# Kernel optimization log

Measured on AMD Instinct MI355X. Metric: run time of the kernel, lower is better.

The kernel has to match this reference:

```python
import jax, jax.numpy as jnp
import numpy as np

B, S, D, H = 4, 2048, 1024, 16
DH = D // H


def setup_inputs() -> dict:
    key = jax.random.key(0)
    k1, k2, k3 = jax.random.split(key, 3)
    x = jax.random.normal(k1, (B, S, D), dtype=jnp.float32)
    w_attn = jax.random.normal(k2, (D, 3 * D), dtype=jnp.float32) * 0.02
    b_attn = jnp.zeros((3 * D,), dtype=jnp.float32)
    w_proj = jax.random.normal(k3, (D, D), dtype=jnp.float32) * 0.02
    b_proj = jnp.zeros((D,), dtype=jnp.float32)
    return {"x": x, "w_attn": w_attn, "b_attn": b_attn, "w_proj": w_proj, "b_proj": b_proj}


def _split_heads(t):
    # [B, S, D] -> [B, H, S, DH]
    return t.reshape(B, S, H, DH).transpose(0, 2, 1, 3)


def reference(x, w_attn, b_attn, w_proj, b_proj):
    # fused QKV projection (TFConv1D = x @ w + b)
    qkv = jnp.einsum('bsd,df->bsf', x, w_attn) + b_attn  # [B, S, 3D]
    q, k, v = jnp.split(qkv, 3, axis=2)
    q, k, v = _split_heads(q), _split_heads(k), _split_heads(v)  # [B,H,S,DH]

    # scaled scores
    w = jnp.einsum('bhqd,bhkd->bhqk', q, k) / jnp.sqrt(jnp.asarray(DH, dtype=q.dtype))

    # causal mask: multiply + additive -10000 trick, as in original
    i = jnp.arange(S)[:, None]
    j = jnp.arange(S)[None, :]
    b = (i >= j).astype(w.dtype)  # nd == ns so i >= j - ns + nd == i >= j
    b = b[None, None]  # [1,1,S,S]
    w = w * b - 10000.0 * (1.0 - b)

    w = jax.nn.softmax(w, axis=-1)
    # attn_pdrop = 0.0 -> dropout is identity (eval)

    a = jnp.einsum('bhqk,bhkd->bhqd', w, v)  # [B,H,S,DH]
    a = a.transpose(0, 2, 1, 3).reshape(B, S, D)  # merge heads
    a = jnp.einsum('bsd,df->bsf', a, w_proj) + b_proj
    # resid_pdrop = 0.0 -> identity
    return a
```

## Files before the change

### kernel.cpp

```cpp
#include <hip/hip_runtime.h>
#include <stdint.h>

typedef __bf16 bf16x8 __attribute__((ext_vector_type(8)));
typedef float  f32x4  __attribute__((ext_vector_type(4)));

#define DEV __device__ __forceinline__

constexpr int Bc = 4, S = 2048, D = 1024, Hh = 16, DH = 64;
constexpr int Kdim = 1024;

DEV unsigned short f2bf(float f) {
    uint32_t u = __builtin_bit_cast(uint32_t, f);
    u += 0x7fff + ((u >> 16) & 1);
    return (unsigned short)(u >> 16);
}
DEV bf16x8 ld8(const unsigned short* p) {
    uint4 u = *(const uint4*)p;
    return __builtin_bit_cast(bf16x8, u);
}
DEV uint4 pack8(float4 a, float4 b) {
    union { uint4 u; unsigned short s[8]; } r;
    r.s[0] = f2bf(a.x); r.s[1] = f2bf(a.y); r.s[2] = f2bf(a.z); r.s[3] = f2bf(a.w);
    r.s[4] = f2bf(b.x); r.s[5] = f2bf(b.y); r.s[6] = f2bf(b.z); r.s[7] = f2bf(b.w);
    return r.u;
}

DEV void gl16(const void* g, void* l) {
    __builtin_amdgcn_global_load_lds((__attribute__((address_space(1))) void*)g,
                                     (__attribute__((address_space(3))) void*)l,
                                     16, 0, 0);
}

__global__ __launch_bounds__(256) void transpose_cvt(const float* __restrict__ in,
                                                     unsigned short* __restrict__ out,
                                                     int rows, int cols) {
    __shared__ float t[32][33];
    int tx = threadIdx.x & 31, ty = threadIdx.x >> 5;
    int c = blockIdx.x * 32 + tx;
    int rbase = blockIdx.y * 32;
    for (int rr = 0; rr < 32; rr += 8)
        t[ty + rr][tx] = in[(size_t)(rbase + ty + rr) * cols + c];
    __syncthreads();
    int orbase = blockIdx.x * 32;
    for (int rr = 0; rr < 32; rr += 8)
        out[(size_t)(orbase + ty + rr) * rows + rbase + tx] = f2bf(t[tx][ty + rr]);
}

__global__ __launch_bounds__(256) void cvt_bf16(const float* __restrict__ in,
                                                unsigned short* __restrict__ out) {
    size_t i = (size_t)blockIdx.x * 256 + threadIdx.x;
    const float4* p = (const float4*)(in + i * 8);
    float4 a = p[0], b = p[1];
    *(uint4*)(out + i * 8) = pack8(a, b);
}

__global__ __launch_bounds__(256) void gemm_bt(const unsigned short* __restrict__ A,
                                               const unsigned short* __restrict__ Bt,
                                               const float* __restrict__ bias,
                                               int mode,
                                               unsigned short* __restrict__ qo,
                                               unsigned short* __restrict__ ko,
                                               unsigned short* __restrict__ vo,
                                               float* __restrict__ outf) {
    __shared__ __align__(16) unsigned short As[2][128 * 64];
    __shared__ __align__(16) unsigned short Bs[2][128 * 64];
    const int tid = threadIdx.x;
    const int wave = tid >> 6, lane = tid & 63, g = lane >> 4, ln = lane & 15;
    const int wm = wave >> 1, wn = wave & 1;
    const int nwg = gridDim.x * gridDim.y;
    const int orig = blockIdx.y * gridDim.x + blockIdx.x;
    const int swz = (orig & 7) * (nwg >> 3) + (orig >> 3);
    const int m0 = (swz / gridDim.x) * 128, n0 = (swz % gridDim.x) * 128;

    f32x4 acc[4][4];
    for (int i = 0; i < 4; i++)
        for (int j = 0; j < 4; j++) acc[i][j] = f32x4{0.f, 0.f, 0.f, 0.f};

#define STAGE_G(buf, k0)                                                            \
    _Pragma("unroll")                                                               \
    for (int c = 0; c < 4; c++) {                                                   \
        int L = c * 4096 + tid * 16;                                                \
        int row = L >> 7;                                                           \
        int colb = (L & 127) ^ ((row & 7) << 4);                                    \
        gl16((const char*)A  + ((size_t)(m0 + row) * Kdim + (k0)) * 2 + colb,       \
             (char*)As[buf] + c * 4096 + wave * 1024);                              \
        gl16((const char*)Bt + ((size_t)(n0 + row) * Kdim + (k0)) * 2 + colb,       \
             (char*)Bs[buf] + c * 4096 + wave * 1024);                              \
    }

    STAGE_G(0, 0);
    asm volatile("s_waitcnt vmcnt(0)" ::: "memory");
    __builtin_amdgcn_s_barrier();
    asm volatile("" ::: "memory");

#pragma unroll 1
    for (int t = 0; t < 16; t++) {
        const int buf = t & 1;
        if (t + 1 < 16) STAGE_G(buf ^ 1, (t + 1) * 64);
        const unsigned short* Asb = As[buf];
        const unsigned short* Bsb = Bs[buf];
#pragma unroll
        for (int kk = 0; kk < 2; kk++) {
            bf16x8 af[4], bfr[4];
#pragma unroll
            for (int u = 0; u < 4; u++) {
                int ra = wm * 64 + u * 16 + ln;
                int rb = wn * 64 + u * 16 + ln;
                int co = kk * 64 + g * 16;
                af[u]  = ld8((const unsigned short*)((const char*)Asb + ra * 128 + (co ^ ((ra & 7) << 4))));
                bfr[u] = ld8((const unsigned short*)((const char*)Bsb + rb * 128 + (co ^ ((rb & 7) << 4))));
            }
#pragma unroll
            for (int mt = 0; mt < 4; mt++)
#pragma unroll
                for (int nt = 0; nt < 4; nt++)
                    acc[mt][nt] = __builtin_amdgcn_mfma_f32_16x16x32_bf16(af[mt], bfr[nt], acc[mt][nt], 0, 0, 0);
        }
        asm volatile("" ::: "memory");
        asm volatile("s_waitcnt vmcnt(0)" ::: "memory");
        __builtin_amdgcn_s_barrier();
        asm volatile("" ::: "memory");
    }
#undef STAGE_G

    for (int mt = 0; mt < 4; mt++)
        for (int nt = 0; nt < 4; nt++)
            for (int r = 0; r < 4; r++) {
                int m = m0 + wm * 64 + mt * 16 + g * 4 + r;
                int n = n0 + wn * 64 + nt * 16 + ln;
                float val = acc[mt][nt][r] + bias[n];
                if (mode == 0) {
                    int which = n >> 10, rem = n & 1023;
                    int hh = rem >> 6, dd = rem & 63;
                    int b = m >> 11, s = m & 2047;
                    int bh = (b << 4) + hh;
                    if (which == 0)      qo[((size_t)bh * S + s) * DH + dd] = f2bf(val);
                    else if (which == 1) ko[((size_t)bh * S + s) * DH + dd] = f2bf(val);
                    else                 vo[((size_t)bh * DH + dd) * S + s] = f2bf(val);
                } else {
                    outf[(size_t)m * 1024 + n] = val;
                }
            }
}

__global__ __launch_bounds__(512, 4) void attn_fwd(const unsigned short* __restrict__ qg,
                                                   const unsigned short* __restrict__ kg,
                                                   const unsigned short* __restrict__ vtg,
                                                   unsigned short* __restrict__ og) {
    __shared__ __align__(16) unsigned short Ks[128 * 64];
    __shared__ __align__(16) unsigned short Vs[64 * 128];
    __shared__ __align__(16) unsigned short P [128 * 136];
    const int idx = blockIdx.x;
    const int qt = 15 - (idx >> 6);
    const int bh = idx & 63;
    const int b = bh >> 4, h = bh & 15;
    const size_t base = (size_t)bh * S * DH;
    const unsigned short* qp = qg + base;
    const char* kpb  = (const char*)(kg  + base);
    const char* vtpb = (const char*)(vtg + base);
    const int tid = threadIdx.x, wave = tid >> 6, lane = tid & 63;
    const int g = lane >> 4, ln = lane & 15;
    const int q0 = qt * 128, wq = wave * 16;
    const int jn = qt + 1;

    bf16x8 qf[2];
    qf[0] = ld8(qp + (size_t)(q0 + wq + ln) * DH + g * 8);
    qf[1] = ld8(qp + (size_t)(q0 + wq + ln) * DH + 32 + g * 8);

    f32x4 o_t[4];
#pragma unroll
    for (int dt = 0; dt < 4; dt++) o_t[dt] = f32x4{0.f, 0.f, 0.f, 0.f};
    float m_ = -1e30f, l_ = 0.f;

#pragma unroll 1
    for (int j = 0; j < jn; j++) {
        const char* kj = kpb + (size_t)j * (128 * DH * 2);
        const char* vj = vtpb + j * 256;
#pragma unroll
        for (int c = 0; c < 2; c++) {
            int L = c * 8192 + tid * 16;
            int kr = L >> 7, kcb = L & 127;
            gl16(kj + (size_t)kr * 128 + (kcb ^ ((kr & 7) << 4)),
                 (char*)Ks + c * 8192 + wave * 1024);
            int vr = L >> 8, vcb = L & 255;
            gl16(vj + (size_t)vr * 4096 + (vcb ^ ((vr & 15) << 4)),
                 (char*)Vs + c * 8192 + wave * 1024);
        }
        __syncthreads();

        f32x4 st[8];
#pragma unroll
        for (int mt = 0; mt < 8; mt++) {
            int row = mt * 16 + ln;
            int sw = (row & 7) << 4;
            const char* kb2 = (const char*)Ks + row * 128;
            bf16x8 kf0 = ld8((const unsigned short*)(kb2 + ((g * 16) ^ sw)));
            bf16x8 kf1 = ld8((const unsigned short*)(kb2 + ((64 + g * 16) ^ sw)));
            f32x4 t = f32x4{0.f, 0.f, 0.f, 0.f};
            t = __builtin_amdgcn_mfma_f32_16x16x32_bf16(kf0, qf[0], t, 0, 0, 0);
            t = __builtin_amdgcn_mfma_f32_16x16x32_bf16(kf1, qf[1], t, 0, 0, 0);
            st[mt] = t;
        }
        if (j == jn - 1) {
            int qgl = q0 + wq + ln;
#pragma unroll
            for (int mt = 0; mt < 8; mt++)
#pragma unroll
                for (int r = 0; r < 4; r++) {
                    int kvg = j * 128 + mt * 16 + g * 4 + r;
                    if (kvg > qgl) st[mt][r] = -3e38f;
                }
        }
        f32x4 mm = st[0];
#pragma unroll
        for (int mt = 1; mt < 8; mt++)
#pragma unroll
            for (int e = 0; e < 4; e++) mm[e] = fmaxf(mm[e], st[mt][e]);
        float mx = fmaxf(fmaxf(mm[0], mm[1]), fmaxf(mm[2], mm[3]));
        mx = fmaxf(mx, __shfl_xor(mx, 16));
        mx = fmaxf(mx, __shfl_xor(mx, 32));
        float mnew = fmaxf(m_, mx);
        float alpha = __expf((m_ - mnew) * 0.125f);
        f32x4 sv = f32x4{0.f, 0.f, 0.f, 0.f};
#pragma unroll
        for (int mt = 0; mt < 8; mt++) {
            f32x4 pr;
#pragma unroll
            for (int e = 0; e < 4; e++) pr[e] = __expf((st[mt][e] - mnew) * 0.125f);
            st[mt] = pr;
            sv += pr;
        }
        float rs = (sv[0] + sv[1]) + (sv[2] + sv[3]);
        rs += __shfl_xor(rs, 16);
        rs += __shfl_xor(rs, 32);
        l_ = l_ * alpha + rs;
        m_ = mnew;

#pragma unroll
        for (int mt = 0; mt < 8; mt++) {
            uint4 u = __builtin_bit_cast(uint4, st[mt]);
            uint2 w;
            w.x = (u.y & 0xFFFF0000u) | (u.x >> 16);
            w.y = (u.w & 0xFFFF0000u) | (u.z >> 16);
            *(uint2*)&P[(wq + ln) * 136 + mt * 16 + g * 4] = w;
        }
#pragma unroll
        for (int dt = 0; dt < 4; dt++) o_t[dt] *= alpha;

#pragma unroll
        for (int kc = 0; kc < 4; kc++) {
            bf16x8 pf = ld8(&P[(wq + ln) * 136 + kc * 32 + g * 8]);
            bf16x8 vf[4];
#pragma unroll
            for (int dt = 0; dt < 4; dt++) {
                int row = dt * 16 + ln;
                vf[dt] = ld8((const unsigned short*)((const char*)Vs + row * 256 +
                             ((kc * 64 + g * 16) ^ ((row & 15) << 4))));
            }
#pragma unroll
            for (int dt = 0; dt < 4; dt++)
                o_t[dt] = __builtin_amdgcn_mfma_f32_16x16x32_bf16(vf[dt], pf, o_t[dt], 0, 0, 0);
        }
        __syncthreads();
    }

    float il = 1.f / l_;
#pragma unroll
    for (int dt = 0; dt < 4; dt++) o_t[dt] *= il;
    float* Ot = (float*)&P[wq * 136];
#pragma unroll
    for (int dt = 0; dt < 4; dt++)
        *(float4*)&Ot[ln * 68 + dt * 16 + g * 4] =
            float4{o_t[dt][0], o_t[dt][1], o_t[dt][2], o_t[dt][3]};
#pragma unroll
    for (int i = 0; i < 4; i++) {
        float4 v = *(float4*)&Ot[(i * 4 + g) * 68 + ln * 4];
        uint2 w;
        w.x = (uint32_t)f2bf(v.x) | ((uint32_t)f2bf(v.y) << 16);
        w.y = (uint32_t)f2bf(v.z) | ((uint32_t)f2bf(v.w) << 16);
        *(uint2*)&og[((size_t)(b * S + q0 + wq + i * 4 + g)) * D + h * DH + ln * 4] = w;
    }
}

extern "C" void kernel_launch(void* const* d_in, const int* in_sizes, int n_in,
                              void* d_out, int out_size, void* d_ws, size_t ws_size,
                              hipStream_t stream) {
    (void)in_sizes; (void)n_in; (void)out_size; (void)ws_size;
    const float* x      = (const float*)d_in[0];
    const float* w_attn = (const float*)d_in[1];
    const float* b_attn = (const float*)d_in[2];
    const float* w_proj = (const float*)d_in[3];
    const float* b_proj = (const float*)d_in[4];

    char* ws = (char*)d_ws;
    unsigned short* wattn_t = (unsigned short*)ws;
    unsigned short* wproj_t = (unsigned short*)(ws + 6291456);
    unsigned short* xb      = (unsigned short*)(ws + 8388608);
    unsigned short* qb      = (unsigned short*)(ws + 25165824);
    unsigned short* kb      = (unsigned short*)(ws + 41943040);
    unsigned short* vtb     = (unsigned short*)(ws + 58720256);
    unsigned short* aob     = (unsigned short*)(ws + 75497472);

    transpose_cvt<<<dim3(96, 32), 256, 0, stream>>>(w_attn, wattn_t, 1024, 3072);
    transpose_cvt<<<dim3(32, 32), 256, 0, stream>>>(w_proj, wproj_t, 1024, 1024);
    cvt_bf16<<<dim3(4096), 256, 0, stream>>>(x, xb);
    gemm_bt<<<dim3(24, 64), 256, 0, stream>>>(xb, wattn_t, b_attn, 0, qb, kb, vtb, nullptr);
    attn_fwd<<<dim3(1024), 512, 0, stream>>>(qb, kb, vtb, aob);
    gemm_bt<<<dim3(8, 64), 256, 0, stream>>>(aob, wproj_t, b_proj, 1,
                                             nullptr, nullptr, nullptr, (float*)d_out);
}
```

Measured before the change: 264.5 us.

## Restructure GEMM into 128x256 tiles with 8 waves and triple-buffered split staging

The GEMM tile grows from 128x128 with 4 waves to 128x256 with 8 waves, and LDS moves to a triple buffer that prefetches two K-steps ahead. The B-tile global loads are split into two halves issued at different points in the iteration, and each MFMA phase is wrapped in s_setprio. The aim is to hide global-load latency and raise MFMA density per barrier. In exchange the block uses more LDS (144KB), the grid shrinks to half as many blocks (especially small for the projection GEMM: 256 blocks), and the vmcnt bookkeeping becomes delicate.

```diff
diff --git a/kernel.cpp b/kernel.cpp
--- a/kernel.cpp
+++ b/kernel.cpp
@@ -54,81 +54,142 @@
     *(uint4*)(out + i * 8) = pack8(a, b);
 }
 
-__global__ __launch_bounds__(256) void gemm_bt(const unsigned short* __restrict__ A,
-                                               const unsigned short* __restrict__ Bt,
-                                               const float* __restrict__ bias,
-                                               int mode,
-                                               unsigned short* __restrict__ qo,
-                                               unsigned short* __restrict__ ko,
-                                               unsigned short* __restrict__ vo,
-                                               float* __restrict__ outf) {
-    __shared__ __align__(16) unsigned short As[2][128 * 64];
-    __shared__ __align__(16) unsigned short Bs[2][128 * 64];
+__global__ __launch_bounds__(512, 2) void gemm_bt(const unsigned short* __restrict__ A,
+                                                  const unsigned short* __restrict__ Bt,
+                                                  const float* __restrict__ bias,
+                                                  int mode,
+                                                  unsigned short* __restrict__ qo,
+                                                  unsigned short* __restrict__ ko,
+                                                  unsigned short* __restrict__ vo,
+                                                  float* __restrict__ outf) {
+    __shared__ __align__(16) unsigned short As[3][128 * 64];
+    __shared__ __align__(16) unsigned short Bs[3][256 * 64];
     const int tid = threadIdx.x;
     const int wave = tid >> 6, lane = tid & 63, g = lane >> 4, ln = lane & 15;
-    const int wm = wave >> 1, wn = wave & 1;
+    const int wm = wave >> 2, wn = wave & 3;
     const int nwg = gridDim.x * gridDim.y;
     const int orig = blockIdx.y * gridDim.x + blockIdx.x;
     const int swz = (orig & 7) * (nwg >> 3) + (orig >> 3);
-    const int m0 = (swz / gridDim.x) * 128, n0 = (swz % gridDim.x) * 128;
+    const int m0 = (swz / gridDim.x) * 128, n0 = (swz % gridDim.x) * 256;
 
     f32x4 acc[4][4];
     for (int i = 0; i < 4; i++)
         for (int j = 0; j < 4; j++) acc[i][j] = f32x4{0.f, 0.f, 0.f, 0.f};
 
-#define STAGE_G(buf, k0)                                                            \
+#define STAGE_A(buf, k0)                                                            \
     _Pragma("unroll")                                                               \
-    for (int c = 0; c < 4; c++) {                                                   \
-        int L = c * 4096 + tid * 16;                                                \
+    for (int c = 0; c < 2; c++) {                                                   \
+        int L = c * 8192 + tid * 16;                                                \
         int row = L >> 7;                                                           \
         int colb = (L & 127) ^ ((row & 7) << 4);                                    \
-        gl16((const char*)A  + ((size_t)(m0 + row) * Kdim + (k0)) * 2 + colb,       \
-             (char*)As[buf] + c * 4096 + wave * 1024);                              \
+        gl16((const char*)A + ((size_t)(m0 + row) * Kdim + (k0)) * 2 + colb,        \
+             (char*)As[buf] + c * 8192 + wave * 1024);                              \
+    }
+#define STAGE_B01(buf, k0)                                                          \
+    _Pragma("unroll")                                                               \
+    for (int c = 0; c < 2; c++) {                                                   \
+        int L = c * 8192 + tid * 16;                                                \
+        int row = L >> 7;                                                           \
+        int colb = (L & 127) ^ ((row & 7) << 4);                                    \
         gl16((const char*)Bt + ((size_t)(n0 + row) * Kdim + (k0)) * 2 + colb,       \
-             (char*)Bs[buf] + c * 4096 + wave * 1024);                              \
-    }
-
-    STAGE_G(0, 0);
-    asm volatile("s_waitcnt vmcnt(0)" ::: "memory");
+             (char*)Bs[buf] + c * 8192 + wave * 1024);                              \
+    }
+#define STAGE_B23(buf, k0)                                                          \
+    _Pragma("unroll")                                                               \
+    for (int c = 2; c < 4; c++) {                                                   \
+        int L = c * 8192 + tid * 16;                                                \
+        int row = L >> 7;                                                           \
+        int colb = (L & 127) ^ ((row & 7) << 4);                                    \
+        gl16((const char*)Bt + ((size_t)(n0 + row) * Kdim + (k0)) * 2 + colb,       \
+             (char*)Bs[buf] + c * 8192 + wave * 1024);                              \
+    }
+
+    STAGE_A(0, 0);  STAGE_B01(0, 0);  STAGE_B23(0, 0);
+    STAGE_A(1, 64); STAGE_B01(1, 64); STAGE_B23(1, 64);
+    asm volatile("s_waitcnt vmcnt(6)" ::: "memory");
     __builtin_amdgcn_s_barrier();
     asm volatile("" ::: "memory");
 
 #pragma unroll 1
     for (int t = 0; t < 16; t++) {
-        const int buf = t & 1;
-        if (t + 1 < 16) STAGE_G(buf ^ 1, (t + 1) * 64);
-        const unsigned short* Asb = As[buf];
-        const unsigned short* Bsb = Bs[buf];
-#pragma unroll
-        for (int kk = 0; kk < 2; kk++) {
-            bf16x8 af[4], bfr[4];
-#pragma unroll
-            for (int u = 0; u < 4; u++) {
-                int ra = wm * 64 + u * 16 + ln;
-                int rb = wn * 64 + u * 16 + ln;
+        const unsigned short* Asb = As[t % 3];
+        const unsigned short* Bsb = Bs[t % 3];
+        const int bufn = (t + 2) % 3;
+        const int k2 = (t + 2) * 64;
+
+        if (t + 2 < 16) { STAGE_A(bufn, k2); STAGE_B01(bufn, k2); }
+        bf16x8 bfr[4][2];
+#pragma unroll
+        for (int v = 0; v < 4; v++)
+#pragma unroll
+            for (int kk = 0; kk < 2; kk++) {
+                int rb = wn * 64 + v * 16 + ln;
                 int co = kk * 64 + g * 16;
-                af[u]  = ld8((const unsigned short*)((const char*)Asb + ra * 128 + (co ^ ((ra & 7) << 4))));
-                bfr[u] = ld8((const unsigned short*)((const char*)Bsb + rb * 128 + (co ^ ((rb & 7) << 4))));
+                bfr[v][kk] = ld8((const unsigned short*)((const char*)Bsb + rb * 128 + (co ^ ((rb & 7) << 4))));
             }
-#pragma unroll
-            for (int mt = 0; mt < 4; mt++)
-#pragma unroll
-                for (int nt = 0; nt < 4; nt++)
-                    acc[mt][nt] = __builtin_amdgcn_mfma_f32_16x16x32_bf16(af[mt], bfr[nt], acc[mt][nt], 0, 0, 0);
-        }
-        asm volatile("" ::: "memory");
-        asm volatile("s_waitcnt vmcnt(0)" ::: "memory");
+        {
+            bf16x8 af[2][2];
+#pragma unroll
+            for (int u = 0; u < 2; u++)
+#pragma unroll
+                for (int kk = 0; kk < 2; kk++) {
+                    int ra = wm * 64 + u * 16 + ln;
+                    int co = kk * 64 + g * 16;
+                    af[u][kk] = ld8((const unsigned short*)((const char*)Asb + ra * 128 + (co ^ ((ra & 7) << 4))));
+                }
+            __builtin_amdgcn_s_setprio(1);
+#pragma unroll
+            for (int kk = 0; kk < 2; kk++)
+#pragma unroll
+                for (int u = 0; u < 2; u++)
+#pragma unroll
+                    for (int v = 0; v < 4; v++)
+                        acc[u][v] = __builtin_amdgcn_mfma_f32_16x16x32_bf16(af[u][kk], bfr[v][kk], acc[u][v], 0, 0, 0);
+            __builtin_amdgcn_s_setprio(0);
+        }
         __builtin_amdgcn_s_barrier();
         asm volatile("" ::: "memory");
-    }
-#undef STAGE_G
+
+        if (t + 2 < 16) { STAGE_B23(bufn, k2); }
+        {
+            bf16x8 af[2][2];
+#pragma unroll
+            for (int u = 0; u < 2; u++)
+#pragma unroll
+                for (int kk = 0; kk < 2; kk++) {
+                    int ra = wm * 64 + 32 + u * 16 + ln;
+                    int co = kk * 64 + g * 16;
+                    af[u][kk] = ld8((const unsigned short*)((const char*)Asb + ra * 128 + (co ^ ((ra & 7) << 4))));
+                }
+            __builtin_amdgcn_s_setprio(1);
+#pragma unroll
+            for (int kk = 0; kk < 2; kk++)
+#pragma unroll
+                for (int u = 0; u < 2; u++)
+#pragma unroll
+                    for (int v = 0; v < 4; v++)
+                        acc[2 + u][v] = __builtin_amdgcn_mfma_f32_16x16x32_bf16(af[u][kk], bfr[v][kk], acc[2 + u][v], 0, 0, 0);
+            __builtin_amdgcn_s_setprio(0);
+        }
+        asm volatile("" ::: "memory");
+
+        if (t + 1 < 16) {
+            if (t + 2 < 16) asm volatile("s_waitcnt vmcnt(6)" ::: "memory");
+            else            asm volatile("s_waitcnt vmcnt(0)" ::: "memory");
+            __builtin_amdgcn_s_barrier();
+            asm volatile("" ::: "memory");
+        }
+    }
+#undef STAGE_A
+#undef STAGE_B01
+#undef STAGE_B23
 
     for (int mt = 0; mt < 4; mt++)
-        for (int nt = 0; nt < 4; nt++)
+        for (int v = 0; v < 4; v++)
             for (int r = 0; r < 4; r++) {
-                int m = m0 + wm * 64 + mt * 16 + g * 4 + r;
-                int n = n0 + wn * 64 + nt * 16 + ln;
-                float val = acc[mt][nt][r] + bias[n];
+                int m = m0 + wm * 64 + (mt >> 1) * 32 + (mt & 1) * 16 + g * 4 + r;
+                int n = n0 + wn * 64 + v * 16 + ln;
+                float val = acc[mt][v][r] + bias[n];
                 if (mode == 0) {
                     int which = n >> 10, rem = n & 1023;
                     int hh = rem >> 6, dd = rem & 63;
@@ -304,8 +365,8 @@
     transpose_cvt<<<dim3(96, 32), 256, 0, stream>>>(w_attn, wattn_t, 1024, 3072);
     transpose_cvt<<<dim3(32, 32), 256, 0, stream>>>(w_proj, wproj_t, 1024, 1024);
     cvt_bf16<<<dim3(4096), 256, 0, stream>>>(x, xb);
-    gemm_bt<<<dim3(24, 64), 256, 0, stream>>>(xb, wattn_t, b_attn, 0, qb, kb, vtb, nullptr);
+    gemm_bt<<<dim3(12, 64), 512, 0, stream>>>(xb, wattn_t, b_attn, 0, qb, kb, vtb, nullptr);
     attn_fwd<<<dim3(1024), 512, 0, stream>>>(qb, kb, vtb, aob);
-    gemm_bt<<<dim3(8, 64), 256, 0, stream>>>(aob, wproj_t, b_proj, 1,
+    gemm_bt<<<dim3(4, 64), 512, 0, stream>>>(aob, wproj_t, b_proj, 1,
                                              nullptr, nullptr, nullptr, (float*)d_out);
 }
```

After: 302.1 us. 1.14x slower.
